# Kernel tuning notes

Measured on AMD Instinct MI355X. Metric: run time of the kernel, lower is better.

## Reference

```python
import jax, jax.numpy as jnp
import numpy as np


def setup_inputs() -> dict:
    key = jax.random.key(0)
    n_symbols, code_length = 2, 16
    n_types, batch_size = 256, 128
    n_all = n_symbols ** code_length  # 65536 codes
    # enumerate full binary code space as one-hot [A, L, S]
    bits = (np.arange(n_all)[:, None] >> np.arange(code_length - 1, -1, -1)) & 1
    all_codes = np.eye(n_symbols, dtype=np.float32)[bits]
    # source distribution, sorted descending (abundant words first), normalized
    pi = jax.random.uniform(key, (n_types,), dtype=jnp.float32) + 0.1
    pi = jnp.sort(pi)[::-1]
    pi = pi / pi.sum()
    return {
        "pi_t": pi,
        "all_codes_als": jnp.asarray(all_codes),
        "code_length": code_length,
        "n_types": n_types,
        "batch_size": batch_size,
        "two_body_max_n_interactions": 32,
        "top_proposals_per_column": 1024,
        "random_proposals_per_column": 256,
    }


def reference(pi_t, all_codes_als, code_length, n_types, batch_size,
              two_body_max_n_interactions, top_proposals_per_column,
              random_proposals_per_column):
    A, L, S = all_codes_als.shape
    B, T = batch_size, n_types
    P = min(top_proposals_per_column, A)
    R = min(random_proposals_per_column, A)
    W = min(two_body_max_n_interactions, T - 1)  # 'earlier' dropout window
    dt = pi_t.dtype
    base_key = jax.random.key(42)

    # one-body potential: abundance-weighted quadratic on code hamming weight
    w_a = all_codes_als[:, :, 1].sum(-1)  # [A] hamming weight of each code
    type_rank_t = jnp.arange(T, dtype=dt) / T

    def one_body(pi, type_rank):
        target = code_length * (1.0 - type_rank)
        return pi * (w_a - target) ** 2 / code_length  # [A]

    win_off = jnp.arange(W)

    def step(c_btls, i_p):
        i_t = i_p  # sweep_order is identity
        ob_a = one_body(pi_t[i_t], type_rank_t[i_t])
        # top proposals by lowest one-body energy + random proposals (fixed K)
        _, top_idx = jax.lax.top_k(-ob_a, P)
        kr = jax.random.fold_in(base_key, i_p)
        k_rand, k_samp = jax.random.split(kr)
        rand_idx = jax.random.randint(k_rand, (R,), 0, A)
        idx_k = jnp.concatenate([top_idx, rand_idx])  # [K = P + R]
        codes_kls = all_codes_als[idx_k]               # [K, L, S]
        ob_k = ob_a[idx_k]                             # [K]
        # two-body over fixed window of up to W previous columns ('earlier')
        win = i_p - W + win_off                        # [W] previous columns
        valid = (win >= 0).astype(dt)
        win_c = jnp.clip(win, 0, T - 1)
        c2_bwls = jnp.take(c_btls, win_c, axis=1)      # [B, W, L, S]
        overlap_bkw = jnp.einsum('kls,bwls->bkw', codes_kls, c2_bwls)
        pi_w = pi_t[win_c] * valid                     # [W]
        tb_bk = pi_t[i_t] * (overlap_bkw * pi_w[None, None, :]).sum(-1)
        i_pf = i_p.astype(dt)
        n_int = jnp.minimum(i_pf, jnp.asarray(W, dt))
        factor = jnp.where(i_pf > 0, i_pf / jnp.maximum(n_int, 1.0), 0.0)
        two_body_bk = factor * tb_bk                   # dropout compensation
        unnorm_bk = -(ob_k[None, :] + two_body_bk)     # [B, K]
        log_prob_bk = jax.nn.log_softmax(unnorm_bk, axis=-1)
        # action_policy == 'sampled'
        c_b = jax.random.categorical(k_samp, log_prob_bk, axis=-1)  # [B]
        c_btls = c_btls.at[:, i_t].set(codes_kls[c_b])
        lp_b = jnp.take_along_axis(log_prob_bk, c_b[:, None], axis=-1)[:, 0]
        return c_btls, lp_b

    c0 = jnp.zeros((B, T, L, S), dtype=dt)
    c_btls, lp_tb = jax.lax.scan(step, c0, jnp.arange(T))
    log_prob_b = lp_tb.mean(0)  # mean over columns, matching torch cat+mean
    return c_btls, log_prob_b
```

## Files before the change

kernel.cpp:

```cpp
#include <hip/hip_runtime.h>
#include <stdint.h>
#include <math.h>


#define JAX_PARTITIONABLE 1

#define T_COLS 256
#define B_ROWS 128
#define KC     1280
#define PTOP   1024
#define RRAND  256
#define WWIN   32
#define NCAND  20
#define NWAVES 4
#define NCPL   5
#define BLOCK_S 1024
#define NWAVE_S (BLOCK_S / 64)

__device__ __constant__ int dC[17][17] = {
  {1},
  {1,1},
  {1,2,1},
  {1,3,3,1},
  {1,4,6,4,1},
  {1,5,10,10,5,1},
  {1,6,15,20,15,6,1},
  {1,7,21,35,35,21,7,1},
  {1,8,28,56,70,56,28,8,1},
  {1,9,36,84,126,126,84,36,9,1},
  {1,10,45,120,210,252,210,120,45,10,1},
  {1,11,55,165,330,462,462,330,165,55,11,1},
  {1,12,66,220,495,792,924,792,495,220,66,12,1},
  {1,13,78,286,715,1287,1716,1716,1287,715,286,78,13,1},
  {1,14,91,364,1001,2002,3003,3432,3003,2002,1001,364,91,14,1},
  {1,15,105,455,1365,3003,5005,6435,6435,5005,3003,1365,455,105,15,1},
  {1,16,120,560,1820,4368,8008,11440,12870,11440,8008,4368,1820,560,120,16,1}
};

__device__ __forceinline__ void tf_block(uint32_t k0, uint32_t k1,
                                         uint32_t x0, uint32_t x1,
                                         uint32_t& o0, uint32_t& o1) {
  uint32_t ks2 = k0 ^ k1 ^ 0x1BD11BDAu;
  x0 += k0; x1 += k1;
#define TFR(r) { x0 += x1; x1 = (x1 << (r)) | (x1 >> (32 - (r))); x1 ^= x0; }
  TFR(13) TFR(15) TFR(26) TFR(6)   x0 += k1;  x1 += ks2 + 1u;
  TFR(17) TFR(29) TFR(16) TFR(24)  x0 += ks2; x1 += k0 + 2u;
  TFR(13) TFR(15) TFR(26) TFR(6)   x0 += k0;  x1 += k1 + 3u;
  TFR(17) TFR(29) TFR(16) TFR(24)  x0 += k1;  x1 += ks2 + 4u;
  TFR(13) TFR(15) TFR(26) TFR(6)   x0 += ks2; x1 += k0 + 5u;
#undef TFR
  o0 = x0; o1 = x1;
}

__device__ __forceinline__ void derive_keys(int step,
                                            uint32_t* krand, uint32_t* ksamp,
                                            uint32_t* k2) {
  uint32_t y0, y1;
  tf_block(0u, 42u, 0u, (uint32_t)step, y0, y1);
  uint32_t kr0 = y0, kr1 = y1;
#if JAX_PARTITIONABLE
  uint32_t r0, r1;
  tf_block(kr0, kr1, 0u, 0u, r0, r1);
  if (krand) { krand[0] = r0; krand[1] = r1; }
  if (ksamp) { tf_block(kr0, kr1, 0u, 1u, y0, y1); ksamp[0] = y0; ksamp[1] = y1; }
  if (k2)    { tf_block(r0, r1, 0u, 1u, y0, y1);  k2[0] = y0;  k2[1] = y1; }
#else
  uint32_t a0,a1,b0,b1;
  tf_block(kr0, kr1, 0u, 2u, a0, a1);
  tf_block(kr0, kr1, 1u, 3u, b0, b1);
  if (krand) { krand[0] = a0; krand[1] = b0; }
  if (ksamp) { ksamp[0] = a1; ksamp[1] = b1; }
  if (k2) {
    uint32_t c0,c1,d0,d1;
    tf_block(a0, b0, 0u, 2u, c0, c1);
    tf_block(a0, b0, 1u, 3u, d0, d1);
    k2[0] = c1; k2[1] = d1;
  }
#endif
}

__device__ __forceinline__ float gumbel_from_bits(uint32_t bits) {
  uint32_t fb = (bits >> 9) | 0x3f800000u;
  float f = __uint_as_float(fb) - 1.0f;
  float u = (f == 0.0f) ? 1.17549435e-38f : f;
  float l1 = (float)log((double)u);
  float l2 = (float)log((double)(-l1));
  return -l2;
}

__device__ __forceinline__ float gumbel_at(uint32_t ks0, uint32_t ks1, uint32_t j) {
  uint32_t g0, g1;
#if JAX_PARTITIONABLE
  tf_block(ks0, ks1, 0u, j, g0, g1);
  return gumbel_from_bits(g0 ^ g1);
#else
  uint32_t half = (uint32_t)(B_ROWS * KC / 2);
  if (j < half) { tf_block(ks0, ks1, j, j + half, g0, g1);  return gumbel_from_bits(g0); }
  else          { tf_block(ks0, ks1, j - half, j, g0, g1);  return gumbel_from_bits(g1); }
#endif
}

__global__ void __launch_bounds__(256)
gumbel_kernel(float* __restrict__ gw) {
  const int bb   = blockIdx.x & (B_ROWS - 1);
  const int step = blockIdx.x >> 7;
  const int tid  = threadIdx.x;
  __shared__ uint32_t s_ks[2];
  if (tid == 0) {
    uint32_t ks[2];
    derive_keys(step, nullptr, ks, nullptr);
    s_ks[0] = ks[0]; s_ks[1] = ks[1];
  }
  __syncthreads();
  const uint32_t ks0 = s_ks[0], ks1 = s_ks[1];
  const size_t base = ((size_t)bb * T_COLS + step) * KC;
#pragma unroll
  for (int i = 0; i < 5; ++i) {
    int k = tid + 256 * i;
    uint32_t j = (uint32_t)(bb * KC + k);
    gw[base + k] = gumbel_at(ks0, ks1, j);
  }
}

__global__ void __launch_bounds__(256)
cand_kernel(unsigned short* __restrict__ candg) {
  const int step = blockIdx.x;
  const int tid  = threadIdx.x;
  __shared__ int s_dC[17][17];
  __shared__ int s_gw0[17], s_gw1[17], s_gbase[17];
  __shared__ int s_ngrp;
  __shared__ uint32_t s_k2[2];
  for (int i = tid; i < 289; i += 256) s_dC[i/17][i%17] = dC[i/17][i%17];
  if (tid == 0) {
    uint32_t k2[2];
    derive_keys(step, nullptr, nullptr, k2);
    s_k2[0] = k2[0]; s_k2[1] = k2[1];
    int ws[17], am[17];
    for (int w = 0; w < 17; ++w) {
      int m = 16 * w - 256 + step;
      am[w] = m < 0 ? -m : m;
      ws[w] = w;
    }
    for (int a2 = 1; a2 < 17; ++a2) {
      int wv = ws[a2], kv = am[wv];
      int j2 = a2 - 1;
      while (j2 >= 0 && am[ws[j2]] > kv) { ws[j2 + 1] = ws[j2]; --j2; }
      ws[j2 + 1] = wv;
    }
    int ng = 0, base = 0, idx = 0;
    while (idx < 17) {
      int w0 = ws[idx]; int a0v = am[w0]; int w1 = -1;
      if (idx + 1 < 17 && am[ws[idx + 1]] == a0v) { w1 = ws[idx + 1]; ++idx; }
      ++idx;
      s_gw0[ng] = w0; s_gw1[ng] = w1; s_gbase[ng] = base;
      base += dC[16][w0] + (w1 >= 0 ? dC[16][w1] : 0);
      ++ng;
      if (base >= PTOP) break;
    }
    s_ngrp = ng;
  }
  __syncthreads();
  for (int p = tid; p < PTOP; p += 256) {
    int g = 0;
    for (int t2 = 1; t2 < s_ngrp; ++t2) if (s_gbase[t2] <= p) g = t2;
    int q  = p - s_gbase[g];
    int r0 = s_gw0[g], r1 = s_gw1[g];
    uint32_t code = 0;
    for (int pos = 15; pos >= 0; --pos) {
      int n0 = ((r0 >= 0 && r0 <= pos) ? s_dC[pos][r0] : 0)
             + ((r1 >= 0 && r1 <= pos) ? s_dC[pos][r1] : 0);
      if (q >= n0) { q -= n0; code |= (1u << pos); --r0; if (r1 >= 0) --r1; }
    }
    candg[step * KC + p] = (unsigned short)code;
  }
  {
    int t2 = tid;
    uint32_t a0, a1;
#if JAX_PARTITIONABLE
    tf_block(s_k2[0], s_k2[1], 0u, (uint32_t)t2, a0, a1);
    candg[step * KC + PTOP + t2] = (unsigned short)((a0 ^ a1) & 0xFFFFu);
#else
    if (t2 < 128) { tf_block(s_k2[0], s_k2[1], (uint32_t)t2, (uint32_t)(128 + t2), a0, a1);
                    candg[step * KC + PTOP + t2] = (unsigned short)(a0 & 0xFFFFu); }
    else          { tf_block(s_k2[0], s_k2[1], (uint32_t)(t2 - 128), (uint32_t)t2, a0, a1);
                    candg[step * KC + PTOP + t2] = (unsigned short)(a1 & 0xFFFFu); }
#endif
  }
}

__device__ __forceinline__ unsigned pl_down32_u(unsigned x) {
  unsigned d = x, s = x;
  asm volatile("s_nop 1\n\tv_permlane32_swap_b32 %0, %1" : "+v"(d), "+v"(s));
  return s;
}
__device__ __forceinline__ unsigned pl_down16_u(unsigned x) {
  unsigned d = x, s = x;
  asm volatile("s_nop 1\n\tv_permlane16_swap_b32 %0, %1" : "+v"(d), "+v"(s));
  return s;
}
template<int N>
__device__ __forceinline__ unsigned dpp_shl_u(unsigned x) {
  return (unsigned)__builtin_amdgcn_update_dpp(0, (int)x, 0x100 | N, 0xF, 0xF, true);
}
__device__ __forceinline__ float pl_down32_f(float x) {
  return __uint_as_float(pl_down32_u(__float_as_uint(x)));
}
__device__ __forceinline__ float pl_down16_f(float x) {
  return __uint_as_float(pl_down16_u(__float_as_uint(x)));
}
template<int N>
__device__ __forceinline__ float dpp_shl_f(float x) {
  return __uint_as_float(dpp_shl_u<N>(__float_as_uint(x)));
}
__device__ __forceinline__ double pl_down32_d(double x) {
  unsigned lo = pl_down32_u((unsigned)__double2loint(x));
  unsigned hi = pl_down32_u((unsigned)__double2hiint(x));
  return __hiloint2double((int)hi, (int)lo);
}
__device__ __forceinline__ double pl_down16_d(double x) {
  unsigned lo = pl_down16_u((unsigned)__double2loint(x));
  unsigned hi = pl_down16_u((unsigned)__double2hiint(x));
  return __hiloint2double((int)hi, (int)lo);
}
template<int N>
__device__ __forceinline__ double dpp_shl_d(double x) {
  unsigned lo = dpp_shl_u<N>((unsigned)__double2loint(x));
  unsigned hi = dpp_shl_u<N>((unsigned)__double2hiint(x));
  return __hiloint2double((int)hi, (int)lo);
}
__device__ __forceinline__ float bcast0_f(float x) {
  return __uint_as_float((unsigned)__builtin_amdgcn_readfirstlane((int)__float_as_uint(x)));
}
__device__ __forceinline__ int bcast0_i(int x) {
  return __builtin_amdgcn_readfirstlane(x);
}
__device__ __forceinline__ double bcast0_d(double x) {
  int lo = __builtin_amdgcn_readfirstlane(__double2loint(x));
  int hi = __builtin_amdgcn_readfirstlane(__double2hiint(x));
  return __hiloint2double(hi, lo);
}

#define LGKM_BAR()                                                            \
  do {                                                                        \
    asm volatile("s_waitcnt lgkmcnt(0)" ::: "memory");                        \
    __builtin_amdgcn_s_barrier();                                             \
  } while (0)

#define STEP_BODY4(S, CC, GG, CN, GN)                                         \
  {                                                                           \
    const int step = (S);                                                     \
        \
    const int sn = (step + 1 < T_COLS) ? step + 1 : step;                     \
    _Pragma("unroll")                                                         \
    for (int i = 0; i < NCPL; ++i) {                                          \
      CN[i] = candg[sn * KC + (NCPL * wid + i) * 64 + lane];                  \
      GN[i] = gw[gb + (size_t)sn * KC + (NCPL * wid + i) * 64 + lane];        \
    }                                                                         \
             \
    if (lane < 16) {                                                          \
      if (step > 0) {                                                         \
        double pw = (double)s_pi[step - 1];                                   \
        if ((c_last >> lane) & 1u) p1_d += pw;                                \
        pt_d += pw;                                                           \
      }                                                                       \
      if (step >= 33) {                                                       \
        double pw = (double)s_pi[step - 33];                                  \
        if (((uint32_t)s_cint[step - 33] >> lane) & 1u) p1_d -= pw;           \
        pt_d -= pw;                                                           \
      }                                                                       \
    }                                                                         \
    float Dl = (float)(pt_d - (p1_d + p1_d));                                 \
      \
    double s0d = p1_d;                                                        \
    s0d += dpp_shl_d<1>(s0d);                                                 \
    s0d += dpp_shl_d<2>(s0d);                                                 \
    s0d += dpp_shl_d<4>(s0d);                                                 \
    s0d += dpp_shl_d<8>(s0d);                                                 \
    const float S0f  = bcast0_f((float)s0d);                                  \
    const float Pt16 = bcast0_f((float)(16.0 * pt_d));                        \
    {                                                                         \
                 \
      int n = lane >> 4, v = lane & 15;                                       \
      float d0 = __shfl(Dl, 4 * n + 0);                                       \
      float d1 = __shfl(Dl, 4 * n + 1);                                       \
      float d2 = __shfl(Dl, 4 * n + 2);                                       \
      float d3 = __shfl(Dl, 4 * n + 3);                                       \
      float t = 0.0f;                                                         \
      if (v & 1) t += d0;                                                     \
      if (v & 2) t += d1;                                                     \
      if (v & 4) t += d2;                                                     \
      if (v & 8) t += d3;                                                     \
      s_T[n][v] = t;                                                          \
    }                                                                         \
    __builtin_amdgcn_wave_barrier();                                          \
    const float pi_i   = s_pi[step];                                          \
    const float i_pf   = (float)step;                                         \
    const float factor = (step > 0) ? (i_pf / fminf(i_pf, 32.0f)) : 0.0f;     \
    float un[NCPL];                                                           \
    _Pragma("unroll")                                                         \
    for (int i = 0; i < NCPL; ++i) {                                          \
      uint32_t c = CC[i];                                                     \
      float sc = S0f + s_T[0][c & 15];                                        \
      sc += s_T[1][(c >> 4) & 15];                                            \
      sc += s_T[2][(c >> 8) & 15];                                            \
      sc += s_T[3][(c >> 12) & 15];                                           \
      float sv = Pt16 - sc;                                                   \
      int w = __popc(c);                                                      \
      int m = 16 * w - 256 + step;                                            \
      float sq  = (float)(m * m) * 0.00390625f;                               \
      float obk = (pi_i * sq) * 0.0625f;                                      \
      un[i] = -(obk + factor * (pi_i * sv));                                  \
    }                                                                         \
             \
    float wmw = fmaxf(fmaxf(fmaxf(un[0], un[1]), fmaxf(un[2], un[3])),        \
                      un[4]);                                                 \
    s_cf[wid][lane] = wmw;                                                    \
    LGKM_BAR();                                                               \
    float wm = fmaxf(fmaxf(s_cf[0][lane], s_cf[1][lane]),                     \
                     fmaxf(s_cf[2][lane], s_cf[3][lane]));                    \
    wm = fmaxf(wm, pl_down32_f(wm));                                          \
    wm = fmaxf(wm, pl_down16_f(wm));                                          \
    wm = fmaxf(wm, dpp_shl_f<8>(wm));                                         \
    wm = fmaxf(wm, dpp_shl_f<4>(wm));                                         \
    wm = fmaxf(wm, dpp_shl_f<2>(wm));                                         \
    wm = fmaxf(wm, dpp_shl_f<1>(wm));                                         \
    wm = bcast0_f(wm);                                                        \
                      \
    double a0 = 0.0, a1 = 0.0;                                                \
    _Pragma("unroll")                                                         \
    for (int i = 0; i < NCPL; ++i) {                                          \
      float e = expf(un[i] - wm);                                             \
      if ((NCPL * wid + i) & 1) a1 += (double)e; else a0 += (double)e;        \
    }                                                                         \
    s_cd[wid][lane] = a0 + a1;                                                \
    LGKM_BAR();                                                               \
    double sw = ((s_cd[0][lane] + s_cd[1][lane]) + s_cd[2][lane])             \
                + s_cd[3][lane];                                              \
    sw += pl_down32_d(sw);                                                    \
    sw += pl_down16_d(sw);                                                    \
    sw += dpp_shl_d<8>(sw);                                                   \
    sw += dpp_shl_d<4>(sw);                                                   \
    sw += dpp_shl_d<2>(sw);                                                   \
    sw += dpp_shl_d<1>(sw);                                                   \
    const float lsum = logf((float)bcast0_d(sw));                             \
                                        \
    float bz; int bi; float bu;                                               \
    {                                                                         \
      bz = ((un[0] - wm) - lsum) + GG[0];                                     \
      bi = ((64 * (NCPL * wid) + lane) << 16) | (int)CC[0];                   \
      bu = un[0];                                                             \
      _Pragma("unroll")                                                       \
      for (int i = 1; i < NCPL; ++i) {                                        \
        float zi = ((un[i] - wm) - lsum) + GG[i];                             \
        int   ii = ((64 * (NCPL * wid + i) + lane) << 16) | (int)CC[i];       \
        if (zi > bz || (zi == bz && ii < bi)) { bz = zi; bi = ii; bu = un[i]; }\
      }                                                                       \
    }                                                                         \
    s_cz[wid][lane] = bz; s_ci[wid][lane] = bi; s_cu[wid][lane] = bu;         \
    LGKM_BAR();                                                               \
    bz = s_cz[0][lane]; bi = s_ci[0][lane]; bu = s_cu[0][lane];               \
    _Pragma("unroll")                                                         \
    for (int w = 1; w < NWAVES; ++w) {                                        \
      float oz = s_cz[w][lane]; int oi = s_ci[w][lane];                       \
      float ou = s_cu[w][lane];                                               \
      if (oz > bz || (oz == bz && oi < bi)) { bz = oz; bi = oi; bu = ou; }    \
    }                                                                         \
    {                                                                         \
      float oz = pl_down32_f(bz); int oi = (int)pl_down32_u((unsigned)bi);    \
      float ou = pl_down32_f(bu);                                             \
      if (oz > bz || (oz == bz && oi < bi)) { bz = oz; bi = oi; bu = ou; }    \
    }                                                                         \
    {                                                                         \
      float oz = pl_down16_f(bz); int oi = (int)pl_down16_u((unsigned)bi);    \
      float ou = pl_down16_f(bu);                                             \
      if (oz > bz || (oz == bz && oi < bi)) { bz = oz; bi = oi; bu = ou; }    \
    }                                                                         \
    {                                                                         \
      float oz = dpp_shl_f<8>(bz); int oi = (int)dpp_shl_u<8>((unsigned)bi);  \
      float ou = dpp_shl_f<8>(bu);                                            \
      if (oz > bz || (oz == bz && oi < bi)) { bz = oz; bi = oi; bu = ou; }    \
    }                                                                         \
    {                                                                         \
      float oz = dpp_shl_f<4>(bz); int oi = (int)dpp_shl_u<4>((unsigned)bi);  \
      float ou = dpp_shl_f<4>(bu);                                            \
      if (oz > bz || (oz == bz && oi < bi)) { bz = oz; bi = oi; bu = ou; }    \
    }                                                                         \
    {                                                                         \
      float oz = dpp_shl_f<2>(bz); int oi = (int)dpp_shl_u<2>((unsigned)bi);  \
      float ou = dpp_shl_f<2>(bu);                                            \
      if (oz > bz || (oz == bz && oi < bi)) { bz = oz; bi = oi; bu = ou; }    \
    }                                                                         \
    {                                                                         \
      float oz = dpp_shl_f<1>(bz); int oi = (int)dpp_shl_u<1>((unsigned)bi);  \
      float ou = dpp_shl_f<1>(bu);                                            \
      if (oz > bz || (oz == bz && oi < bi)) { bz = oz; bi = oi; bu = ou; }    \
    }                                                                         \
    int wpk = bcast0_i(bi);                                                   \
    c_last = (uint32_t)wpk & 0xFFFFu;                                         \
    if (wid == 0 && lane == 0) {                                              \
      s_cint[step] = (unsigned short)c_last;                                  \
      lp_acc += (double)((bu - wm) - lsum);                                   \
    }                                                                         \
  }

__global__ void __launch_bounds__(256, 1)
mrf_seq_wave4(const float* __restrict__ pi, float* __restrict__ out,
              const float* __restrict__ gw,
              const unsigned short* __restrict__ candg) {
#pragma clang fp contract(off)
  const int b    = blockIdx.x;
  const int tid  = threadIdx.x;
  const int lane = tid & 63;
  const int wid  = tid >> 6;
  const size_t gb = (size_t)b * T_COLS * KC;

  __shared__ float          s_pi[T_COLS];
  __shared__ unsigned short s_cint[T_COLS];
  __shared__ float          s_T[4][16];
  __shared__ float          s_cf[NWAVES][64];
  __shared__ double         s_cd[NWAVES][64];
  __shared__ float          s_cz[NWAVES][64];
  __shared__ int            s_ci[NWAVES][64];
  __shared__ float          s_cu[NWAVES][64];

  for (int t = tid; t < T_COLS; t += 256) s_pi[t] = pi[t];
  __syncthreads();

  double lp_acc = 0.0;
  uint32_t c_last = 0;
  double p1_d = 0.0, pt_d = 0.0;

  float    gA[NCPL], gB[NCPL];
  uint32_t cA[NCPL], cB[NCPL];
#pragma unroll
  for (int i = 0; i < NCPL; ++i) {
    cA[i] = candg[(NCPL * wid + i) * 64 + lane];
    gA[i] = gw[gb + (NCPL * wid + i) * 64 + lane];
  }

  for (int s2 = 0; s2 < T_COLS; s2 += 2) {
    STEP_BODY4(s2,     cA, gA, cB, gB)
    STEP_BODY4(s2 + 1, cB, gB, cA, gA)
  }

  __syncthreads();
  for (int idx2 = tid; idx2 < T_COLS * 32; idx2 += 256) {
    int t    = idx2 >> 5;
    int rem  = idx2 & 31;
    int l    = rem >> 1;
    int sbit = rem & 1;
    uint32_t code = s_cint[t];
    int bit = (int)((code >> (15 - l)) & 1u);
    out[(size_t)b * 8192 + idx2] = (float)(sbit ? bit : (1 - bit));
  }
  if (tid == 0) {
    out[(size_t)B_ROWS * 8192 + b] = (float)(lp_acc / 256.0);
  }
}

template<int MODE>
__global__ void __launch_bounds__(BLOCK_S)
mrf_seq_kernel(const float* __restrict__ pi, float* __restrict__ out,
               const float* __restrict__ gw,
               const unsigned short* __restrict__ candg) {
#pragma clang fp contract(off)
  const int b    = blockIdx.x;
  const int tid  = threadIdx.x;
  const bool has1 = tid < (KC - BLOCK_S);

  __shared__ float          s_pi[T_COLS];
  __shared__ unsigned short s_cand[KC];
  __shared__ float          s_unnorm[KC];
  __shared__ unsigned short s_cint[T_COLS];
  __shared__ int            s_dC[17][17];
  __shared__ int            s_gw0[17], s_gw1[17], s_gbase[17];
  __shared__ int            s_ngrp;
  __shared__ uint32_t       s_keys[6];
  __shared__ float          s_pw[WWIN];
  __shared__ unsigned short s_wc[WWIN];
  __shared__ float          s_redf[NWAVE_S];
  __shared__ double         s_redd[NWAVE_S];
  __shared__ int            s_redi[NWAVE_S];
  __shared__ float          s_bcast[2];

  for (int t = tid; t < T_COLS; t += BLOCK_S) s_pi[t] = pi[t];
  if (MODE == 0) {
    for (int i = tid; i < 289; i += BLOCK_S) s_dC[i/17][i%17] = dC[i/17][i%17];
  }
  double lp_acc = 0.0;
  __syncthreads();

  for (int step = 0; step < T_COLS; ++step) {
    if (MODE <= 1 && tid == 0) {
      if (MODE == 1) {
        uint32_t ks[2];
        derive_keys(step, nullptr, ks, nullptr);
        s_keys[2] = ks[0]; s_keys[3] = ks[1];
      } else {
        uint32_t ks[2], k2[2];
        derive_keys(step, nullptr, ks, k2);
        s_keys[2] = ks[0]; s_keys[3] = ks[1];
        s_keys[4] = k2[0]; s_keys[5] = k2[1];
        int ws[17], am[17];
        for (int w = 0; w < 17; ++w) {
          int m = 16 * w - 256 + step;
          am[w] = m < 0 ? -m : m;
          ws[w] = w;
        }
        for (int a2 = 1; a2 < 17; ++a2) {
          int wvv = ws[a2], kv = am[wvv];
          int j2 = a2 - 1;
          while (j2 >= 0 && am[ws[j2]] > kv) { ws[j2 + 1] = ws[j2]; --j2; }
          ws[j2 + 1] = wvv;
        }
        int ng = 0, base = 0, idx = 0;
        while (idx < 17) {
          int w0 = ws[idx]; int a0v = am[w0]; int w1 = -1;
          if (idx + 1 < 17 && am[ws[idx + 1]] == a0v) { w1 = ws[idx + 1]; ++idx; }
          ++idx;
          s_gw0[ng] = w0; s_gw1[ng] = w1; s_gbase[ng] = base;
          base += dC[16][w0] + (w1 >= 0 ? dC[16][w1] : 0);
          ++ng;
          if (base >= PTOP) break;
        }
        s_ngrp = ng;
      }
    }
    if (tid < WWIN) {
      int win = step - WWIN + tid;
      s_pw[tid] = (win >= 0) ? s_pi[win] : 0.0f;
      s_wc[tid] = (win >= 0) ? s_cint[win] : (unsigned short)0;
    }
    __syncthreads();

    uint32_t c0, c1 = 0;
    if (MODE >= 1) {
      c0 = candg[step * KC + tid];
      if (has1) c1 = candg[step * KC + BLOCK_S + tid];
    } else {
      {
        int p = tid;
        int g = 0;
        for (int t2 = 1; t2 < s_ngrp; ++t2) if (s_gbase[t2] <= p) g = t2;
        int q  = p - s_gbase[g];
        int r0 = s_gw0[g], r1 = s_gw1[g];
        uint32_t code = 0;
        for (int pos = 15; pos >= 0; --pos) {
          int n0 = ((r0 >= 0 && r0 <= pos) ? s_dC[pos][r0] : 0)
                 + ((r1 >= 0 && r1 <= pos) ? s_dC[pos][r1] : 0);
          if (q >= n0) { q -= n0; code |= (1u << pos); --r0; if (r1 >= 0) --r1; }
        }
        c0 = code;
      }
      if (has1) {
        int t2 = tid;
        uint32_t a0, a1;
#if JAX_PARTITIONABLE
        tf_block(s_keys[4], s_keys[5], 0u, (uint32_t)t2, a0, a1);
        c1 = (a0 ^ a1) & 0xFFFFu;
#else
        if (t2 < 128) { tf_block(s_keys[4], s_keys[5], (uint32_t)t2, (uint32_t)(128 + t2), a0, a1);
                        c1 = a0 & 0xFFFFu; }
        else          { tf_block(s_keys[4], s_keys[5], (uint32_t)(t2 - 128), (uint32_t)t2, a0, a1);
                        c1 = a1 & 0xFFFFu; }
#endif
      }
    }
    s_cand[tid] = (unsigned short)c0;
    if (has1) s_cand[BLOCK_S + tid] = (unsigned short)c1;

    const float pi_i   = s_pi[step];
    const float i_pf   = (float)step;
    const float factor = (step > 0) ? (i_pf / fminf(i_pf, 32.0f)) : 0.0f;

    float un0, un1 = -3.402823466e+38f;
    {
      int w = __popc(c0);
      int m = 16 * w - 256 + step;
      float sq  = (float)(m * m) * 0.00390625f;
      float obk = (pi_i * sq) * 0.0625f;
      float s = 0.0f;
      for (int w2 = 0; w2 < WWIN; ++w2) {
        float ov = (float)(16 - __popc(c0 ^ (uint32_t)s_wc[w2]));
        s = s + s_pw[w2] * ov;
      }
      un0 = -(obk + factor * (pi_i * s));
    }
    if (has1) {
      int w = __popc(c1);
      int m = 16 * w - 256 + step;
      float sq  = (float)(m * m) * 0.00390625f;
      float obk = (pi_i * sq) * 0.0625f;
      float s = 0.0f;
      for (int w2 = 0; w2 < WWIN; ++w2) {
        float ov = (float)(16 - __popc(c1 ^ (uint32_t)s_wc[w2]));
        s = s + s_pw[w2] * ov;
      }
      un1 = -(obk + factor * (pi_i * s));
    }
    s_unnorm[tid] = un0;
    if (has1) s_unnorm[BLOCK_S + tid] = un1;

    float g0v = 0.0f, g1v = 0.0f;
    if (MODE == 2) {
      const size_t gbase = ((size_t)b * T_COLS + step) * KC;
      g0v = gw[gbase + tid];
      if (has1) g1v = gw[gbase + BLOCK_S + tid];
    } else {
      const uint32_t ks0 = s_keys[2], ks1 = s_keys[3];
      g0v = gumbel_at(ks0, ks1, (uint32_t)(b * KC + tid));
      if (has1) g1v = gumbel_at(ks0, ks1, (uint32_t)(b * KC + BLOCK_S + tid));
    }

    float pmax = has1 ? fmaxf(un0, un1) : un0;
    for (int off = 32; off > 0; off >>= 1) pmax = fmaxf(pmax, __shfl_down(pmax, off));
    if ((tid & 63) == 0) s_redf[tid >> 6] = pmax;
    __syncthreads();
    if (tid == 0) {
      float mm = s_redf[0];
      for (int w2 = 1; w2 < NWAVE_S; ++w2) mm = fmaxf(mm, s_redf[w2]);
      s_bcast[0] = mm;
    }
    __syncthreads();
    const float rmax = s_bcast[0];

    double acc = (double)((float)exp((double)(un0 - rmax)));
    if (has1) acc += (double)((float)exp((double)(un1 - rmax)));
    for (int off = 32; off > 0; off >>= 1) acc += __shfl_down(acc, off);
    if ((tid & 63) == 0) s_redd[tid >> 6] = acc;
    __syncthreads();
    if (tid == 0) {
      double ss = 0.0;
      for (int w2 = 0; w2 < NWAVE_S; ++w2) ss += s_redd[w2];
      float sum_f = (float)ss;
      s_bcast[1] = (float)log((double)sum_f);
    }
    __syncthreads();
    const float lsum = s_bcast[1];

    float bz = ((un0 - rmax) - lsum) + g0v;
    int   bi = tid;
    if (has1) {
      float z1 = ((un1 - rmax) - lsum) + g1v;
      if (z1 > bz) { bz = z1; bi = BLOCK_S + tid; }
    }
    for (int off = 32; off > 0; off >>= 1) {
      float oz = __shfl_down(bz, off);
      int   oi = __shfl_down(bi, off);
      if (oz > bz || (oz == bz && oi < bi)) { bz = oz; bi = oi; }
    }
    if ((tid & 63) == 0) { s_redf[tid >> 6] = bz; s_redi[tid >> 6] = bi; }
    __syncthreads();
    if (tid == 0) {
      float bz2 = s_redf[0]; int bi2 = s_redi[0];
      for (int w2 = 1; w2 < NWAVE_S; ++w2) {
        if (s_redf[w2] > bz2 || (s_redf[w2] == bz2 && s_redi[w2] < bi2)) {
          bz2 = s_redf[w2]; bi2 = s_redi[w2];
        }
      }
      s_cint[step] = s_cand[bi2];
      float lpw = (s_unnorm[bi2] - rmax) - lsum;
      lp_acc += (double)lpw;
    }
    __syncthreads();
  }

  for (int idx2 = tid; idx2 < T_COLS * 32; idx2 += BLOCK_S) {
    int t    = idx2 >> 5;
    int rem  = idx2 & 31;
    int l    = rem >> 1;
    int sbit = rem & 1;
    uint32_t code = s_cint[t];
    int bit = (int)((code >> (15 - l)) & 1u);
    out[(size_t)b * 8192 + idx2] = (float)(sbit ? bit : (1 - bit));
  }
  if (tid == 0) {
    out[(size_t)B_ROWS * 8192 + b] = (float)(lp_acc / 256.0);
  }
}

extern "C" void kernel_launch(void* const* d_in, const int* in_sizes, int n_in,
                              void* d_out, int out_size, void* d_ws, size_t ws_size,
                              hipStream_t stream) {
  const float* pi = (const float*)d_in[0];
  float* out = (float*)d_out;

  const size_t cand_bytes = (size_t)T_COLS * KC * sizeof(unsigned short);
  const size_t gw_bytes   = (size_t)B_ROWS * T_COLS * KC * sizeof(float);

  if (ws_size >= cand_bytes + gw_bytes) {
    unsigned short* candg = (unsigned short*)d_ws;
    float* gw = (float*)((char*)d_ws + cand_bytes);
    gumbel_kernel<<<dim3(T_COLS * B_ROWS), dim3(256), 0, stream>>>(gw);
    cand_kernel<<<dim3(T_COLS), dim3(256), 0, stream>>>(candg);
    mrf_seq_wave4<<<dim3(B_ROWS), dim3(256), 0, stream>>>(pi, out, gw, candg);
  } else if (ws_size >= cand_bytes) {
    unsigned short* candg = (unsigned short*)d_ws;
    cand_kernel<<<dim3(T_COLS), dim3(256), 0, stream>>>(candg);
    mrf_seq_kernel<1><<<dim3(B_ROWS), dim3(BLOCK_S), 0, stream>>>(pi, out, nullptr, candg);
  } else {
    mrf_seq_kernel<0><<<dim3(B_ROWS), dim3(BLOCK_S), 0, stream>>>(pi, out, nullptr, nullptr);
  }
}
```

Baseline: 879.4 us.

## Fuse Gumbel noise generation into sequential kernel via producer waves and LDS double-buffer

Drops the separate kernel that materialized the full per-row, per-step Gumbel noise tensor in global memory. The sequential sampling kernel now runs 8 waves: 4 consumer waves do the per-step sampling, and 4 producer waves compute the next step's Gumbel values into a double-buffered LDS array, kept in step by matching barriers. This removes a large global write and the matching reads, at the cost of extra register and LDS pressure and tighter barrier coupling inside the latency-bound step loop.

```diff
diff --git a/kernel.cpp b/kernel.cpp
--- a/kernel.cpp
+++ b/kernel.cpp
@@ -101,28 +101,6 @@
 }
 
 __global__ void __launch_bounds__(256)
-gumbel_kernel(float* __restrict__ gw) {
-  const int bb   = blockIdx.x & (B_ROWS - 1);
-  const int step = blockIdx.x >> 7;
-  const int tid  = threadIdx.x;
-  __shared__ uint32_t s_ks[2];
-  if (tid == 0) {
-    uint32_t ks[2];
-    derive_keys(step, nullptr, ks, nullptr);
-    s_ks[0] = ks[0]; s_ks[1] = ks[1];
-  }
-  __syncthreads();
-  const uint32_t ks0 = s_ks[0], ks1 = s_ks[1];
-  const size_t base = ((size_t)bb * T_COLS + step) * KC;
-#pragma unroll
-  for (int i = 0; i < 5; ++i) {
-    int k = tid + 256 * i;
-    uint32_t j = (uint32_t)(bb * KC + k);
-    gw[base + k] = gumbel_at(ks0, ks1, j);
-  }
-}
-
-__global__ void __launch_bounds__(256)
 cand_kernel(unsigned short* __restrict__ candg) {
   const int step = blockIdx.x;
   const int tid  = threadIdx.x;
@@ -246,16 +224,19 @@
     __builtin_amdgcn_s_barrier();                                             \
   } while (0)
 
-#define STEP_BODY4(S, CC, GG, CN, GN)                                         \
-  {                                                                           \
+#define STEP_F(S, CUR, CC, CN)                                                \
+  if (wid < NWAVES) {                                                         \
     const int step = (S);                                                     \
         \
+    float GGl[NCPL];                                                          \
+    _Pragma("unroll")                                                         \
+    for (int i = 0; i < NCPL; ++i)                                            \
+      GGl[i] = s_gg[CUR][(NCPL * wid + i) * 64 + lane];                       \
+                                   \
     const int sn = (step + 1 < T_COLS) ? step + 1 : step;                     \
     _Pragma("unroll")                                                         \
-    for (int i = 0; i < NCPL; ++i) {                                          \
+    for (int i = 0; i < NCPL; ++i)                                            \
       CN[i] = candg[sn * KC + (NCPL * wid + i) * 64 + lane];                  \
-      GN[i] = gw[gb + (size_t)sn * KC + (NCPL * wid + i) * 64 + lane];        \
-    }                                                                         \
              \
     if (lane < 16) {                                                          \
       if (step > 0) {                                                         \
@@ -270,7 +251,6 @@
       }                                                                       \
     }                                                                         \
     float Dl = (float)(pt_d - (p1_d + p1_d));                                 \
-      \
     double s0d = p1_d;                                                        \
     s0d += dpp_shl_d<1>(s0d);                                                 \
     s0d += dpp_shl_d<2>(s0d);                                                 \
@@ -279,7 +259,6 @@
     const float S0f  = bcast0_f((float)s0d);                                  \
     const float Pt16 = bcast0_f((float)(16.0 * pt_d));                        \
     {                                                                         \
-                 \
       int n = lane >> 4, v = lane & 15;                                       \
       float d0 = __shfl(Dl, 4 * n + 0);                                       \
       float d1 = __shfl(Dl, 4 * n + 1);                                       \
@@ -311,7 +290,6 @@
       float obk = (pi_i * sq) * 0.0625f;                                      \
       un[i] = -(obk + factor * (pi_i * sv));                                  \
     }                                                                         \
-             \
     float wmw = fmaxf(fmaxf(fmaxf(un[0], un[1]), fmaxf(un[2], un[3])),        \
                       un[4]);                                                 \
     s_cf[wid][lane] = wmw;                                                    \
@@ -325,7 +303,6 @@
     wm = fmaxf(wm, dpp_shl_f<2>(wm));                                         \
     wm = fmaxf(wm, dpp_shl_f<1>(wm));                                         \
     wm = bcast0_f(wm);                                                        \
-                      \
     double a0 = 0.0, a1 = 0.0;                                                \
     _Pragma("unroll")                                                         \
     for (int i = 0; i < NCPL; ++i) {                                          \
@@ -343,15 +320,14 @@
     sw += dpp_shl_d<2>(sw);                                                   \
     sw += dpp_shl_d<1>(sw);                                                   \
     const float lsum = logf((float)bcast0_d(sw));                             \
-                                        \
     float bz; int bi; float bu;                                               \
     {                                                                         \
-      bz = ((un[0] - wm) - lsum) + GG[0];                                     \
+      bz = ((un[0] - wm) - lsum) + GGl[0];                                    \
       bi = ((64 * (NCPL * wid) + lane) << 16) | (int)CC[0];                   \
       bu = un[0];                                                             \
       _Pragma("unroll")                                                       \
       for (int i = 1; i < NCPL; ++i) {                                        \
-        float zi = ((un[i] - wm) - lsum) + GG[i];                             \
+        float zi = ((un[i] - wm) - lsum) + GGl[i];                            \
         int   ii = ((64 * (NCPL * wid + i) + lane) << 16) | (int)CC[i];       \
         if (zi > bz || (zi == bz && ii < bi)) { bz = zi; bi = ii; bu = un[i]; }\
       }                                                                       \
@@ -401,18 +377,33 @@
       s_cint[step] = (unsigned short)c_last;                                  \
       lp_acc += (double)((bu - wm) - lsum);                                   \
     }                                                                         \
-  }
-
-__global__ void __launch_bounds__(256, 1)
-mrf_seq_wave4(const float* __restrict__ pi, float* __restrict__ out,
-              const float* __restrict__ gw,
-              const unsigned short* __restrict__ candg) {
+  } else {                                                                    \
+                                         \
+    const int SN = (S) + 1;                                                   \
+    if (SN < T_COLS) {                                                        \
+      const int gwid = wid - NWAVES;                                          \
+      const uint32_t k0 = s_ks[SN][0], k1 = s_ks[SN][1];                      \
+      _Pragma("unroll")                                                       \
+      for (int i = 0; i < NCPL; ++i) {                                        \
+        int k = (NCPL * gwid + i) * 64 + lane;                                \
+        s_gg[1 - (CUR)][k] = gumbel_at(k0, k1, (uint32_t)(b * KC + k));       \
+      }                                                                       \
+    }                                                                         \
+    LGKM_BAR();                                                               \
+    LGKM_BAR();                                                               \
+    LGKM_BAR();                                                               \
+  }
+
+__global__ void __launch_bounds__(512, 1)
+mrf_fused4(const float* __restrict__ pi, float* __restrict__ out,
+           const unsigned short* __restrict__ candg) {
 #pragma clang fp contract(off)
   const int b    = blockIdx.x;
   const int tid  = threadIdx.x;
   const int lane = tid & 63;
   const int wid  = tid >> 6;
-  const size_t gb = (size_t)b * T_COLS * KC;
+  const size_t gbKC = (size_t)b * KC;
+  (void)gbKC;
 
   __shared__ float          s_pi[T_COLS];
   __shared__ unsigned short s_cint[T_COLS];
@@ -422,29 +413,46 @@
   __shared__ float          s_cz[NWAVES][64];
   __shared__ int            s_ci[NWAVES][64];
   __shared__ float          s_cu[NWAVES][64];
-
-  for (int t = tid; t < T_COLS; t += 256) s_pi[t] = pi[t];
+  __shared__ float          s_gg[2][KC];
+  __shared__ uint32_t       s_ks[T_COLS][2];
+
+  for (int t = tid; t < T_COLS; t += 512) s_pi[t] = pi[t];
+  if (tid < T_COLS) {
+    uint32_t ks[2];
+    derive_keys(tid, nullptr, ks, nullptr);
+    s_ks[tid][0] = ks[0]; s_ks[tid][1] = ks[1];
+  }
   __syncthreads();
 
   double lp_acc = 0.0;
   uint32_t c_last = 0;
   double p1_d = 0.0, pt_d = 0.0;
 
-  float    gA[NCPL], gB[NCPL];
+  float    dummyG = 0.0f; (void)dummyG;
   uint32_t cA[NCPL], cB[NCPL];
+
+  if (wid >= NWAVES) {
+    const int gwid = wid - NWAVES;
+    const uint32_t k0 = s_ks[0][0], k1 = s_ks[0][1];
 #pragma unroll
-  for (int i = 0; i < NCPL; ++i) {
-    cA[i] = candg[(NCPL * wid + i) * 64 + lane];
-    gA[i] = gw[gb + (NCPL * wid + i) * 64 + lane];
-  }
+    for (int i = 0; i < NCPL; ++i) {
+      int k = (NCPL * gwid + i) * 64 + lane;
+      s_gg[0][k] = gumbel_at(k0, k1, (uint32_t)(b * KC + k));
+    }
+  } else {
+#pragma unroll
+    for (int i = 0; i < NCPL; ++i)
+      cA[i] = candg[(NCPL * wid + i) * 64 + lane];
+  }
+  __syncthreads();
 
   for (int s2 = 0; s2 < T_COLS; s2 += 2) {
-    STEP_BODY4(s2,     cA, gA, cB, gB)
-    STEP_BODY4(s2 + 1, cB, gB, cA, gA)
+    STEP_F(s2,     0, cA, cB)
+    STEP_F(s2 + 1, 1, cB, cA)
   }
 
   __syncthreads();
-  for (int idx2 = tid; idx2 < T_COLS * 32; idx2 += 256) {
+  for (int idx2 = tid; idx2 < T_COLS * 32; idx2 += 512) {
     int t    = idx2 >> 5;
     int rem  = idx2 & 31;
     int l    = rem >> 1;
@@ -602,11 +610,7 @@
     if (has1) s_unnorm[BLOCK_S + tid] = un1;
 
     float g0v = 0.0f, g1v = 0.0f;
-    if (MODE == 2) {
-      const size_t gbase = ((size_t)b * T_COLS + step) * KC;
-      g0v = gw[gbase + tid];
-      if (has1) g1v = gw[gbase + BLOCK_S + tid];
-    } else {
+    {
       const uint32_t ks0 = s_keys[2], ks1 = s_keys[3];
       g0v = gumbel_at(ks0, ks1, (uint32_t)(b * KC + tid));
       if (has1) g1v = gumbel_at(ks0, ks1, (uint32_t)(b * KC + BLOCK_S + tid));
@@ -686,18 +690,11 @@
   float* out = (float*)d_out;
 
   const size_t cand_bytes = (size_t)T_COLS * KC * sizeof(unsigned short);
-  const size_t gw_bytes   = (size_t)B_ROWS * T_COLS * KC * sizeof(float);
-
-  if (ws_size >= cand_bytes + gw_bytes) {
-    unsigned short* candg = (unsigned short*)d_ws;
-    float* gw = (float*)((char*)d_ws + cand_bytes);
-    gumbel_kernel<<<dim3(T_COLS * B_ROWS), dim3(256), 0, stream>>>(gw);
-    cand_kernel<<<dim3(T_COLS), dim3(256), 0, stream>>>(candg);
-    mrf_seq_wave4<<<dim3(B_ROWS), dim3(256), 0, stream>>>(pi, out, gw, candg);
-  } else if (ws_size >= cand_bytes) {
+
+  if (ws_size >= cand_bytes) {
     unsigned short* candg = (unsigned short*)d_ws;
     cand_kernel<<<dim3(T_COLS), dim3(256), 0, stream>>>(candg);
-    mrf_seq_kernel<1><<<dim3(B_ROWS), dim3(BLOCK_S), 0, stream>>>(pi, out, nullptr, candg);
+    mrf_fused4<<<dim3(B_ROWS), dim3(512), 0, stream>>>(pi, out, candg);
   } else {
     mrf_seq_kernel<0><<<dim3(B_ROWS), dim3(BLOCK_S), 0, stream>>>(pi, out, nullptr, nullptr);
   }
```

Result: slower. 947.2 us (+7.7%).
